# Kernel tuning notes

Measured on AMD Instinct MI355X. Metric: run time of the kernel, lower is better.

## Reference

```python
import jax, jax.numpy as jnp
import numpy as np

E, D, H = 1024, 64, 16   # embed_dim, head_dim, num_heads
B, L = 8, 4096


def _ln(x, g, b, eps=1e-5):
    m = jnp.mean(x, axis=-1, keepdims=True)
    v = jnp.var(x, axis=-1, keepdims=True)
    return (x - m) / jnp.sqrt(v + eps) * g + b


def setup_inputs() -> dict:
    key = jax.random.key(0)
    ks = jax.random.split(key, 10)
    s_e = 1.0 / np.sqrt(E)
    s_d = 1.0 / np.sqrt(D)
    f32 = jnp.float32
    return {
        "emb": jax.random.normal(ks[0], (B, L, E), f32),
        # per-head linears stacked on a leading head axis
        "Wa": jax.random.normal(ks[1], (H, E, D), f32) * s_e,
        "ba": jnp.zeros((H, D), f32),
        "Wb": jax.random.normal(ks[2], (H, E, D), f32) * s_e,
        "bb": jnp.zeros((H, D), f32),
        "Wc": jax.random.normal(ks[3], (H, D, D), f32) * s_d,
        "bc": jnp.zeros((H, D), f32),
        "head_w": jnp.ones((H,), f32),
        "hn_g": jnp.ones((H, D), f32),
        "hn_b": jnp.zeros((H, D), f32),
        "Wd": jax.random.normal(ks[4], (E, D), f32) * s_e,
        "bd": jnp.zeros((D,), f32),
        "W1": jax.random.normal(ks[5], (D, 4 * D), f32) * s_d,
        "b1": jnp.zeros((4 * D,), f32),
        "W2": jax.random.normal(ks[6], (4 * D, D), f32) * (1.0 / np.sqrt(4 * D)),
        "b2": jnp.zeros((D,), f32),
        "Wp": jax.random.normal(ks[7], (D, D), f32) * s_d,
        "bp": jnp.zeros((D,), f32),
        "ng": jnp.ones((D,), f32),
        "nb": jnp.zeros((D,), f32),
    }


def reference(emb, Wa, ba, Wb, bb, Wc, bc, head_w, hn_g, hn_b,
              Wd, bd, W1, b1, W2, b2, Wp, bp, ng, nb):
    b_sz, seq_len, _ = emb.shape
    n_heads, d_head = ba.shape

    # gates depend only on x_t -> precompute for all t, all heads  [B,L,H,D]
    a = jnp.tanh(jnp.einsum('ble,hed->blhd', emb, Wa) + ba)
    bt = jnp.einsum('ble,hed->blhd', emb, Wb) + bb

    # linear recurrence h_t = a_t * h_{t-1} + b_t over time
    a_t = jnp.moveaxis(a, 1, 0)    # [L,B,H,D]
    b_t = jnp.moveaxis(bt, 1, 0)

    def step(h, ab):
        at, btt = ab
        h = at * h + btt
        return h, h

    h0 = jnp.zeros((b_sz, n_heads, d_head), emb.dtype)
    _, hs = jax.lax.scan(step, h0, (a_t, b_t))
    hs = jnp.moveaxis(hs, 0, 1)    # [B,L,H,D]

    dx = emb @ Wd + bd             # [B,L,D] shared D(x_t)

    out = jnp.einsum('blhd,hde->blhe', hs, Wc) + bc + dx[:, :, None, :]
    out = _ln(out, hn_g, hn_b)     # per-head LayerNorm, gamma/beta [H,D]

    sum_heads = dx + jnp.einsum('h,blhd->bld', head_w, out)
    z = sum_heads / n_heads

    u = z + _ln(z, ng, nb)
    ffn = jax.nn.gelu(u @ W1 + b1, approximate=False) @ W2 + b2
    h_out = u + ffn
    return h_out @ Wp + bp
```

## Files before the change

### kernel.cpp

```cpp
#include <hip/hip_runtime.h>
#include <hip/hip_bf16.h>
#include <math.h>
#include <stdint.h>

#define E_DIM 1024
#define D_DIM 64
#define H_DIM 16
#define B_SZ  8
#define L_SEQ 4096
#define M_TOK (B_SZ * L_SEQ)
#define NCAT  2112
#define NPAD  2176
#define CHUNK 128
#define NCHUNK (L_SEQ / CHUNK)

typedef float  f32x4  __attribute__((ext_vector_type(4)));
typedef __bf16 bf16x8 __attribute__((ext_vector_type(8)));
typedef __bf16 bf16x4 __attribute__((ext_vector_type(4)));

__device__ __forceinline__ float tanh_fast(float v) {
  float vc = fminf(fmaxf(v, -12.f), 12.f);
  float ex = __expf(vc + vc);
  return (ex - 1.f) / (ex + 1.f);
}
__device__ __forceinline__ void load_lds16(const void* g, void* l) {
  __builtin_amdgcn_global_load_lds(
      (const __attribute__((address_space(1))) void*)g,
      (__attribute__((address_space(3))) void*)l, 16, 0, 0);
}

__global__ __launch_bounds__(256) void prep(
    const float* __restrict__ emb, bf16x4* __restrict__ embh,
    const float* __restrict__ Wa, const float* __restrict__ ba,
    const float* __restrict__ Wb, const float* __restrict__ bb,
    const float* __restrict__ Wd, const float* __restrict__ bd,
    __bf16* __restrict__ wcat, float* __restrict__ bias,
    const float* __restrict__ W1, const float* __restrict__ W2,
    const float* __restrict__ Wp,
    __bf16* __restrict__ g_w1t, __bf16* __restrict__ g_w2t,
    __bf16* __restrict__ g_wpt,
    const float* __restrict__ Wc, __bf16* __restrict__ wct) {
  const int blk = blockIdx.x, tid = threadIdx.x;
  if (blk < 32768) {
    int i = blk * 256 + tid;
    float4 v = ((const float4*)emb)[i];
    bf16x4 o;
    o[0] = (__bf16)v.x; o[1] = (__bf16)v.y; o[2] = (__bf16)v.z; o[3] = (__bf16)v.w;
    embh[i] = o;
  } else if (blk < 41472) {
    int gid = (blk - 32768) * 256 + tid;
    int n = gid >> 10, k = gid & 1023;
    float w, bv;
    if (n < 1024) {
      int h = n >> 6, d = n & 63;
      w = Wa[((h << 10) | k) * 64 + d]; bv = ba[n];
    } else if (n < 2048) {
      int nn = n - 1024; int h = nn >> 6, d = nn & 63;
      w = Wb[((h << 10) | k) * 64 + d]; bv = bb[nn];
    } else if (n < NCAT) {
      int d = n - 2048;
      w = Wd[k * 64 + d];  bv = bd[d];
    } else { w = 0.f; bv = 0.f; }
    wcat[n * 1024 + k] = (__bf16)w;
    if (k == 0) bias[n] = bv;
  } else if (blk < 41616) {
    int idx = (blk - 41472) * 256 + tid;
    if (idx < 16384) {
      int k = idx >> 8, n = idx & 255;
      g_w1t[n * 72 + k] = (__bf16)W1[idx];
    } else if (idx < 32768) {
      int j = idx - 16384; int k = j >> 6, n = j & 63;
      g_w2t[n * 256 + k] = (__bf16)W2[j];
    } else {
      int j = idx - 32768; int k = j >> 6, n = j & 63;
      g_wpt[n * 72 + k] = (__bf16)Wp[j];
    }
  } else {
    int idx = (blk - 41616) * 256 + tid;
    int h = idx >> 12, e = (idx >> 6) & 63, d = idx & 63;
    wct[idx] = (__bf16)Wc[h * 4096 + d * 64 + e];
  }
}

__global__ __launch_bounds__(256) void gemm_fused(
    const __bf16* __restrict__ A, const __bf16* __restrict__ Wt,
    const float* __restrict__ bias,
    __bf16* __restrict__ abuf, __bf16* __restrict__ bbuf, float* __restrict__ dxbuf) {
  __shared__ __bf16 As[128 * 64];
  __shared__ __bf16 Bs[128 * 64];
  const int bb = blockIdx.x;
  const int xcd = bb & 7, wv = bb >> 3;
  const int nt = wv % 17;
  const int mt = xcd * 32 + wv / 17;
  const int m0 = mt * 128, n0 = nt * 128;
  const int t = threadIdx.x, w = t >> 6, l = t & 63;
  const int lr = l >> 3, lc = l & 7;
  const int swz = lc ^ lr;
  const int q = l >> 4, c16 = l & 15;

  f32x4 acc[4][4];
#pragma unroll
  for (int i = 0; i < 4; ++i)
#pragma unroll
    for (int j = 0; j < 4; ++j) acc[i][j] = (f32x4)(0.f);

  const __bf16* gA = A  + (size_t)(m0 + w * 8 + lr) * 1024 + swz * 8;
  const __bf16* gB = Wt + (size_t)(n0 + w * 8 + lr) * 1024 + swz * 8;
  __bf16* lA = As + w * 512;
  __bf16* lB = Bs + w * 512;

  for (int kk = 0; kk < 16; ++kk) {
    const int k0 = kk * 64;
#pragma unroll
    for (int r = 0; r < 4; ++r) {
      load_lds16(gA + (size_t)r * 32 * 1024 + k0, lA + r * 2048);
      load_lds16(gB + (size_t)r * 32 * 1024 + k0, lB + r * 2048);
    }
    __syncthreads();
#pragma unroll
    for (int ks = 0; ks < 2; ++ks) {
      bf16x8 af[4], bfr[4];
#pragma unroll
      for (int i = 0; i < 4; ++i) {
        int mloc = (w >> 1) * 64 + i * 16 + c16;
        int cp = (ks * 4 + q) ^ (mloc & 7);
        af[i] = *(const bf16x8*)(As + mloc * 64 + cp * 8);
      }
#pragma unroll
      for (int j = 0; j < 4; ++j) {
        int nloc = (w & 1) * 64 + j * 16 + c16;
        int cp = (ks * 4 + q) ^ (nloc & 7);
        bfr[j] = *(const bf16x8*)(Bs + nloc * 64 + cp * 8);
      }
#pragma unroll
      for (int i = 0; i < 4; ++i)
#pragma unroll
        for (int j = 0; j < 4; ++j)
          acc[i][j] = __builtin_amdgcn_mfma_f32_16x16x32_bf16(af[i], bfr[j], acc[i][j], 0, 0, 0);
    }
    __syncthreads();
  }

#pragma unroll
  for (int j = 0; j < 4; ++j) {
    int n = n0 + (w & 1) * 64 + j * 16 + c16;
    float bv = bias[n];
#pragma unroll
    for (int i = 0; i < 4; ++i) {
      int mbase = m0 + (w >> 1) * 64 + i * 16 + q * 4;
#pragma unroll
      for (int r = 0; r < 4; ++r) {
        float v = acc[i][j][r] + bv;
        int m = mbase + r;
        if (n < 1024)            abuf[(size_t)m * 1024 + n] = (__bf16)tanh_fast(v);
        else if (n < 2048)       bbuf[(size_t)m * 1024 + (n - 1024)] = (__bf16)v;
        else if (n < NCAT)       dxbuf[m * 64 + (n - 2048)] = v;
      }
    }
  }
}

__global__ __launch_bounds__(256) void scan_local_bf(
    __bf16* __restrict__ abuf, __bf16* __restrict__ bbuf,
    float* __restrict__ cA, float* __restrict__ cH) {
  int bc = blockIdx.x;
  int n4 = threadIdx.x * 4;
  size_t base = (size_t)bc * CHUNK * 1024 + n4;
  float p[4] = {1.f, 1.f, 1.f, 1.f}, h[4] = {0.f, 0.f, 0.f, 0.f};
  for (int s = 0; s < CHUNK; ++s) {
    size_t idx = base + (size_t)s * 1024;
    bf16x4 av = *(const bf16x4*)(abuf + idx);
    bf16x4 bv = *(const bf16x4*)(bbuf + idx);
    bf16x4 po, ho;
#pragma unroll
    for (int i = 0; i < 4; ++i) {
      float a = (float)av[i];
      p[i] *= a;
      h[i] = fmaf(a, h[i], (float)bv[i]);
      po[i] = (__bf16)p[i];
      ho[i] = (__bf16)h[i];
    }
    *(bf16x4*)(abuf + idx) = po;
    *(bf16x4*)(bbuf + idx) = ho;
  }
  int ci = bc * 1024 + n4;
  float4 pv = {p[0], p[1], p[2], p[3]};
  float4 hv = {h[0], h[1], h[2], h[3]};
  *(float4*)(cA + ci) = pv;
  *(float4*)(cH + ci) = hv;
}

__global__ __launch_bounds__(256) void scan_carry(
    const float* __restrict__ cA, const float* __restrict__ cH, float* __restrict__ cIn) {
  int gid = blockIdx.x * 256 + threadIdx.x;
  int n = gid & 1023, b = gid >> 10;
  float carry = 0.f;
  for (int c = 0; c < NCHUNK; ++c) {
    int idx = (b * NCHUNK + c) * 1024 + n;
    cIn[idx] = carry;
    carry = fmaf(cA[idx], carry, cH[idx]);
  }
}

__global__ __launch_bounds__(256) void heads_mfma(
    const __bf16* __restrict__ ahat, const __bf16* __restrict__ hloc,
    const float* __restrict__ dxbuf, const float* __restrict__ cIn,
    const __bf16* __restrict__ wct, const float* __restrict__ bch,
    const float* __restrict__ head_w, const float* __restrict__ hng,
    const float* __restrict__ hnb, const float* __restrict__ ng,
    const float* __restrict__ nbv, float* __restrict__ ubuf) {
  __shared__ float carryS[1024];
  const int tid = threadIdx.x, w = tid >> 6, l = tid & 63;
  const int q = l >> 4, c16 = l & 15;
  const int m0 = blockIdx.x * 64;
  const int b = m0 >> 12, c = (m0 & 4095) >> 7;
  const int cb = (b * NCHUNK + c) * 1024;
  ((float4*)carryS)[tid] = ((const float4*)(cIn + cb))[tid];
  __syncthreads();

  const size_t arow = (size_t)(m0 + w * 16 + c16) * 1024;

  float dxr[4][4];
#pragma unroll
  for (int j = 0; j < 4; ++j)
#pragma unroll
    for (int r = 0; r < 4; ++r)
      dxr[j][r] = dxbuf[(m0 + w * 16 + q * 4 + r) * 64 + j * 16 + c16];

  f32x4 accum[4];
#pragma unroll
  for (int j = 0; j < 4; ++j) accum[j] = (f32x4)(0.f);

  for (int h = 0; h < H_DIM; ++h) {
    bf16x8 af[2];
#pragma unroll
    for (int ks = 0; ks < 2; ++ks) {
      int dbase = h * 64 + ks * 32 + q * 8;
      bf16x8 av = *(const bf16x8*)(ahat + arow + dbase);
      bf16x8 hv = *(const bf16x8*)(hloc + arow + dbase);
      float4 cv0 = *(const float4*)(carryS + dbase);
      float4 cv1 = *(const float4*)(carryS + dbase + 4);
      bf16x8 hf;
      hf[0] = (__bf16)fmaf((float)av[0], cv0.x, (float)hv[0]);
      hf[1] = (__bf16)fmaf((float)av[1], cv0.y, (float)hv[1]);
      hf[2] = (__bf16)fmaf((float)av[2], cv0.z, (float)hv[2]);
      hf[3] = (__bf16)fmaf((float)av[3], cv0.w, (float)hv[3]);
      hf[4] = (__bf16)fmaf((float)av[4], cv1.x, (float)hv[4]);
      hf[5] = (__bf16)fmaf((float)av[5], cv1.y, (float)hv[5]);
      hf[6] = (__bf16)fmaf((float)av[6], cv1.z, (float)hv[6]);
      hf[7] = (__bf16)fmaf((float)av[7], cv1.w, (float)hv[7]);
      af[ks] = hf;
    }
    f32x4 acc[4];
#pragma unroll
    for (int j = 0; j < 4; ++j) acc[j] = (f32x4)(0.f);
#pragma unroll
    for (int ks = 0; ks < 2; ++ks)
#pragma unroll
      for (int j = 0; j < 4; ++j) {
        bf16x8 bf = *(const bf16x8*)(wct + h * 4096 + (j * 16 + c16) * 64 + ks * 32 + q * 8);
        acc[j] = __builtin_amdgcn_mfma_f32_16x16x32_bf16(af[ks], bf, acc[j], 0, 0, 0);
      }
    float hw = head_w[h];
    float g4[4], be4[4], bb4[4];
#pragma unroll
    for (int j = 0; j < 4; ++j) {
      int nh = h * 64 + j * 16 + c16;
      g4[j] = hng[nh]; bb4[j] = hnb[nh]; be4[j] = bch[nh];
    }
#pragma unroll
    for (int r = 0; r < 4; ++r) {
      float v0 = acc[0][r] + be4[0] + dxr[0][r];
      float v1 = acc[1][r] + be4[1] + dxr[1][r];
      float v2 = acc[2][r] + be4[2] + dxr[2][r];
      float v3 = acc[3][r] + be4[3] + dxr[3][r];
      float s  = (v0 + v1) + (v2 + v3);
      float s2 = fmaf(v0, v0, fmaf(v1, v1, fmaf(v2, v2, v3 * v3)));
#pragma unroll
      for (int off = 1; off < 16; off <<= 1) {
        s  += __shfl_xor(s, off, 64);
        s2 += __shfl_xor(s2, off, 64);
      }
      float mean = s * (1.f / 64.f);
      float var  = fmaf(s2, 1.f / 64.f, -mean * mean);
      float inv  = rsqrtf(fmaxf(var, 0.f) + 1e-5f);
      accum[0][r] = fmaf(hw, fmaf((v0 - mean) * inv, g4[0], bb4[0]), accum[0][r]);
      accum[1][r] = fmaf(hw, fmaf((v1 - mean) * inv, g4[1], bb4[1]), accum[1][r]);
      accum[2][r] = fmaf(hw, fmaf((v2 - mean) * inv, g4[2], bb4[2]), accum[2][r]);
      accum[3][r] = fmaf(hw, fmaf((v3 - mean) * inv, g4[3], bb4[3]), accum[3][r]);
    }
  }
  float ng4[4], nb4[4];
#pragma unroll
  for (int j = 0; j < 4; ++j) { ng4[j] = ng[j * 16 + c16]; nb4[j] = nbv[j * 16 + c16]; }
#pragma unroll
  for (int r = 0; r < 4; ++r) {
    float z0 = (dxr[0][r] + accum[0][r]) * (1.f / 16.f);
    float z1 = (dxr[1][r] + accum[1][r]) * (1.f / 16.f);
    float z2 = (dxr[2][r] + accum[2][r]) * (1.f / 16.f);
    float z3 = (dxr[3][r] + accum[3][r]) * (1.f / 16.f);
    float s  = (z0 + z1) + (z2 + z3);
    float s2 = fmaf(z0, z0, fmaf(z1, z1, fmaf(z2, z2, z3 * z3)));
#pragma unroll
    for (int off = 1; off < 16; off <<= 1) {
      s  += __shfl_xor(s, off, 64);
      s2 += __shfl_xor(s2, off, 64);
    }
    float mean = s * (1.f / 64.f);
    float var  = fmaf(s2, 1.f / 64.f, -mean * mean);
    float inv  = rsqrtf(fmaxf(var, 0.f) + 1e-5f);
    int mrow = (m0 + w * 16 + q * 4 + r) * 64;
    ubuf[mrow + 0 * 16 + c16] = z0 + fmaf((z0 - mean) * inv, ng4[0], nb4[0]);
    ubuf[mrow + 1 * 16 + c16] = z1 + fmaf((z1 - mean) * inv, ng4[1], nb4[1]);
    ubuf[mrow + 2 * 16 + c16] = z2 + fmaf((z2 - mean) * inv, ng4[2], nb4[2]);
    ubuf[mrow + 3 * 16 + c16] = z3 + fmaf((z3 - mean) * inv, ng4[3], nb4[3]);
  }
}

__global__ __launch_bounds__(256) void ffn_wave(
    const float* __restrict__ ubuf,
    const __bf16* __restrict__ g_w1t, const __bf16* __restrict__ g_w2t,
    const __bf16* __restrict__ g_wpt,
    const float* __restrict__ b1, const float* __restrict__ b2,
    const float* __restrict__ bp, float* __restrict__ out) {
  __shared__ __bf16 tls[4][4096];
  const int tid = threadIdx.x, w = tid >> 6, l = tid & 63;
  const int q = l >> 4, c16 = l & 15;
  const int m0w = blockIdx.x * 64 + w * 16;
  __bf16* T = tls[w];

  bf16x8 ua[2];
#pragma unroll
  for (int ks = 0; ks < 2; ++ks) {
    const float* up = ubuf + (size_t)(m0w + c16) * 64 + ks * 32 + q * 8;
    float4 v0 = *(const float4*)up;
    float4 v1 = *(const float4*)(up + 4);
    bf16x8 tt;
    tt[0] = (__bf16)v0.x; tt[1] = (__bf16)v0.y; tt[2] = (__bf16)v0.z; tt[3] = (__bf16)v0.w;
    tt[4] = (__bf16)v1.x; tt[5] = (__bf16)v1.y; tt[6] = (__bf16)v1.z; tt[7] = (__bf16)v1.w;
    ua[ks] = tt;
  }

  f32x4 acc1[16];
#pragma unroll
  for (int j = 0; j < 16; ++j) acc1[j] = (f32x4)(0.f);
#pragma unroll
  for (int j = 0; j < 16; ++j) {
    const __bf16* bp1 = g_w1t + (j * 16 + c16) * 72 + q * 8;
    bf16x8 b0 = *(const bf16x8*)bp1;
    bf16x8 b1f = *(const bf16x8*)(bp1 + 32);
    acc1[j] = __builtin_amdgcn_mfma_f32_16x16x32_bf16(ua[0], b0, acc1[j], 0, 0, 0);
    acc1[j] = __builtin_amdgcn_mfma_f32_16x16x32_bf16(ua[1], b1f, acc1[j], 0, 0, 0);
  }

#pragma unroll
  for (int j = 0; j < 16; ++j) {
    int n = j * 16 + c16;
    float bv = b1[n];
#pragma unroll
    for (int rr = 0; rr < 4; ++rr) {
      int tok = q * 4 + rr;
      float x = acc1[j][rr] + bv;
      float g = 0.5f * x * (1.f + erff(x * 0.70710678118654752f));
      T[tok * 256 + (((n >> 3) ^ (tok & 7)) << 3) + (n & 7)] = (__bf16)g;
    }
  }
  __builtin_amdgcn_wave_barrier();

  f32x4 acc2[4];
#pragma unroll
  for (int j = 0; j < 4; ++j) acc2[j] = (f32x4)(0.f);
#pragma unroll
  for (int ks = 0; ks < 8; ++ks) {
    bf16x8 a = *(const bf16x8*)(T + c16 * 256 + (((ks * 4 + q) ^ (c16 & 7)) << 3));
#pragma unroll
    for (int j = 0; j < 4; ++j) {
      bf16x8 b = *(const bf16x8*)(g_w2t + (j * 16 + c16) * 256 + ks * 32 + q * 8);
      acc2[j] = __builtin_amdgcn_mfma_f32_16x16x32_bf16(a, b, acc2[j], 0, 0, 0);
    }
  }
  __builtin_amdgcn_wave_barrier();

#pragma unroll
  for (int j = 0; j < 4; ++j) {
    int e = j * 16 + c16;
    float bv = b2[e];
#pragma unroll
    for (int rr = 0; rr < 4; ++rr) {
      int tok = q * 4 + rr;
      float hres = acc2[j][rr] + bv + ubuf[(size_t)(m0w + tok) * 64 + e];
      T[tok * 64 + (((e >> 3) ^ (tok & 7)) << 3) + (e & 7)] = (__bf16)hres;
    }
  }
  __builtin_amdgcn_wave_barrier();

  f32x4 acc3[4];
#pragma unroll
  for (int j = 0; j < 4; ++j) acc3[j] = (f32x4)(0.f);
#pragma unroll
  for (int ks = 0; ks < 2; ++ks) {
    bf16x8 a = *(const bf16x8*)(T + c16 * 64 + (((ks * 4 + q) ^ (c16 & 7)) << 3));
#pragma unroll
    for (int j = 0; j < 4; ++j) {
      bf16x8 b = *(const bf16x8*)(g_wpt + (j * 16 + c16) * 72 + ks * 32 + q * 8);
      acc3[j] = __builtin_amdgcn_mfma_f32_16x16x32_bf16(a, b, acc3[j], 0, 0, 0);
    }
  }
#pragma unroll
  for (int j = 0; j < 4; ++j) {
    int e = j * 16 + c16;
    float bv = bp[e];
#pragma unroll
    for (int rr = 0; rr < 4; ++rr)
      out[(size_t)(m0w + q * 4 + rr) * 64 + e] = acc3[j][rr] + bv;
  }
}

extern "C" void kernel_launch(void* const* d_in, const int* in_sizes, int n_in,
                              void* d_out, int out_size, void* d_ws, size_t ws_size,
                              hipStream_t stream) {
  const float* emb    = (const float*)d_in[0];
  const float* Wa     = (const float*)d_in[1];
  const float* ba     = (const float*)d_in[2];
  const float* Wb     = (const float*)d_in[3];
  const float* bb     = (const float*)d_in[4];
  const float* Wc     = (const float*)d_in[5];
  const float* bc     = (const float*)d_in[6];
  const float* head_w = (const float*)d_in[7];
  const float* hn_g   = (const float*)d_in[8];
  const float* hn_b   = (const float*)d_in[9];
  const float* Wd     = (const float*)d_in[10];
  const float* bd     = (const float*)d_in[11];
  const float* W1     = (const float*)d_in[12];
  const float* b1     = (const float*)d_in[13];
  const float* W2     = (const float*)d_in[14];
  const float* b2     = (const float*)d_in[15];
  const float* Wp     = (const float*)d_in[16];
  const float* bp     = (const float*)d_in[17];
  const float* ng     = (const float*)d_in[18];
  const float* nb     = (const float*)d_in[19];
  float* out = (float*)d_out;

  char* wsp = (char*)d_ws;
  size_t off = 0;
  auto alloc = [&](size_t bytes) -> char* {
    char* p = wsp + off;
    off += (bytes + 255) & ~(size_t)255;
    return p;
  };
  __bf16* embh  = (__bf16*)alloc((size_t)M_TOK * E_DIM * 2);
  __bf16* wcat  = (__bf16*)alloc((size_t)NPAD * E_DIM * 2);
  float*  bias  = (float*)alloc((size_t)NPAD * 4);
  __bf16* abuf  = (__bf16*)alloc((size_t)M_TOK * 1024 * 2);
  __bf16* bbuf  = (__bf16*)alloc((size_t)M_TOK * 1024 * 2);
  float*  dxbuf = (float*)alloc((size_t)M_TOK * 64 * 4);
  float*  cA    = (float*)alloc((size_t)256 * 1024 * 4);
  float*  cH    = (float*)alloc((size_t)256 * 1024 * 4);
  float*  cIn   = (float*)alloc((size_t)256 * 1024 * 4);
  float*  ubuf  = (float*)alloc((size_t)M_TOK * 64 * 4);
  __bf16* g_w1t = (__bf16*)alloc((size_t)256 * 72 * 2);
  __bf16* g_w2t = (__bf16*)alloc((size_t)64 * 256 * 2);
  __bf16* g_wpt = (__bf16*)alloc((size_t)64 * 72 * 2);
  __bf16* wct   = (__bf16*)alloc((size_t)H_DIM * 64 * 64 * 2);

  prep<<<dim3(41872), dim3(256), 0, stream>>>(
      emb, (bf16x4*)embh, Wa, ba, Wb, bb, Wd, bd, wcat, bias,
      W1, W2, Wp, g_w1t, g_w2t, g_wpt, Wc, wct);
  gemm_fused<<<dim3(4352), dim3(256), 0, stream>>>(embh, wcat, bias, abuf, bbuf, dxbuf);
  scan_local_bf<<<dim3(256), dim3(256), 0, stream>>>(abuf, bbuf, cA, cH);
  scan_carry<<<dim3(32), dim3(256), 0, stream>>>(cA, cH, cIn);
  heads_mfma<<<dim3(512), dim3(256), 0, stream>>>(abuf, bbuf, dxbuf, cIn, wct, bc,
                                                  head_w, hn_g, hn_b, ng, nb, ubuf);
  ffn_wave<<<dim3(512), dim3(256), 0, stream>>>(ubuf, g_w1t, g_w2t, g_wpt,
                                                b1, b2, bp, out);
}
```

Baseline: 610.9 us.

## Fuse carry scan, heads and FFN into one kernel; load GEMM B fragments directly

Removes the scan_carry kernel by having each heads block recompute its chunk carry from the per-chunk (A,H) summaries. It also merges heads_mfma and ffn_wave so the u tensor stays in registers and LDS and never round-trips through global memory. The main GEMM now reads B-operand fragments straight from global memory into registers instead of staging them through LDS, which halves the shared memory used and drops the B-side LDS traffic. The cost is redundant carry work (up to 31 chunk steps per block), more registers per thread in the fused kernel, and B-operand global loads that are no longer shared across waves.

Result: slower. 718.2 us (+17.6%).

```diff
diff --git a/kernel.cpp b/kernel.cpp
--- a/kernel.cpp
+++ b/kernel.cpp
@@ -87,7 +87,6 @@
     const float* __restrict__ bias,
     __bf16* __restrict__ abuf, __bf16* __restrict__ bbuf, float* __restrict__ dxbuf) {
   __shared__ __bf16 As[128 * 64];
-  __shared__ __bf16 Bs[128 * 64];
   const int bb = blockIdx.x;
   const int xcd = bb & 7, wv = bb >> 3;
   const int nt = wv % 17;
@@ -104,22 +103,31 @@
 #pragma unroll
     for (int j = 0; j < 4; ++j) acc[i][j] = (f32x4)(0.f);
 
-  const __bf16* gA = A  + (size_t)(m0 + w * 8 + lr) * 1024 + swz * 8;
-  const __bf16* gB = Wt + (size_t)(n0 + w * 8 + lr) * 1024 + swz * 8;
+  const __bf16* gA = A + (size_t)(m0 + w * 8 + lr) * 1024 + swz * 8;
   __bf16* lA = As + w * 512;
-  __bf16* lB = Bs + w * 512;
+
+  const __bf16* gBj[4];
+#pragma unroll
+  for (int j = 0; j < 4; ++j)
+    gBj[j] = Wt + (size_t)(n0 + (w & 1) * 64 + j * 16 + c16) * 1024 + q * 8;
 
   for (int kk = 0; kk < 16; ++kk) {
     const int k0 = kk * 64;
 #pragma unroll
-    for (int r = 0; r < 4; ++r) {
+    for (int r = 0; r < 4; ++r)
       load_lds16(gA + (size_t)r * 32 * 1024 + k0, lA + r * 2048);
-      load_lds16(gB + (size_t)r * 32 * 1024 + k0, lB + r * 2048);
-    }
+
+    bf16x8 bfr[2][4];
+#pragma unroll
+    for (int ks = 0; ks < 2; ++ks)
+#pragma unroll
+      for (int j = 0; j < 4; ++j)
+        bfr[ks][j] = *(const bf16x8*)(gBj[j] + k0 + ks * 32);
+
     __syncthreads();
 #pragma unroll
     for (int ks = 0; ks < 2; ++ks) {
-      bf16x8 af[4], bfr[4];
+      bf16x8 af[4];
 #pragma unroll
       for (int i = 0; i < 4; ++i) {
         int mloc = (w >> 1) * 64 + i * 16 + c16;
@@ -127,16 +135,10 @@
         af[i] = *(const bf16x8*)(As + mloc * 64 + cp * 8);
       }
 #pragma unroll
-      for (int j = 0; j < 4; ++j) {
-        int nloc = (w & 1) * 64 + j * 16 + c16;
-        int cp = (ks * 4 + q) ^ (nloc & 7);
-        bfr[j] = *(const bf16x8*)(Bs + nloc * 64 + cp * 8);
-      }
-#pragma unroll
       for (int i = 0; i < 4; ++i)
 #pragma unroll
         for (int j = 0; j < 4; ++j)
-          acc[i][j] = __builtin_amdgcn_mfma_f32_16x16x32_bf16(af[i], bfr[j], acc[i][j], 0, 0, 0);
+          acc[i][j] = __builtin_amdgcn_mfma_f32_16x16x32_bf16(af[i], bfr[ks][j], acc[i][j], 0, 0, 0);
     }
     __syncthreads();
   }
@@ -190,32 +192,38 @@
   *(float4*)(cH + ci) = hv;
 }
 
-__global__ __launch_bounds__(256) void scan_carry(
-    const float* __restrict__ cA, const float* __restrict__ cH, float* __restrict__ cIn) {
-  int gid = blockIdx.x * 256 + threadIdx.x;
-  int n = gid & 1023, b = gid >> 10;
-  float carry = 0.f;
-  for (int c = 0; c < NCHUNK; ++c) {
-    int idx = (b * NCHUNK + c) * 1024 + n;
-    cIn[idx] = carry;
-    carry = fmaf(cA[idx], carry, cH[idx]);
-  }
-}
-
-__global__ __launch_bounds__(256) void heads_mfma(
+__global__ __launch_bounds__(256) void heads_ffn(
     const __bf16* __restrict__ ahat, const __bf16* __restrict__ hloc,
-    const float* __restrict__ dxbuf, const float* __restrict__ cIn,
-    const __bf16* __restrict__ wct, const float* __restrict__ bch,
-    const float* __restrict__ head_w, const float* __restrict__ hng,
-    const float* __restrict__ hnb, const float* __restrict__ ng,
-    const float* __restrict__ nbv, float* __restrict__ ubuf) {
+    const float* __restrict__ dxbuf, const float* __restrict__ cA,
+    const float* __restrict__ cH, const __bf16* __restrict__ wct,
+    const float* __restrict__ bch, const float* __restrict__ head_w,
+    const float* __restrict__ hng, const float* __restrict__ hnb,
+    const float* __restrict__ ng, const float* __restrict__ nbv,
+    const __bf16* __restrict__ g_w1t, const __bf16* __restrict__ g_w2t,
+    const __bf16* __restrict__ g_wpt,
+    const float* __restrict__ b1, const float* __restrict__ b2,
+    const float* __restrict__ bp, float* __restrict__ out) {
   __shared__ float carryS[1024];
+  __shared__ __bf16 tls[4][4096];
   const int tid = threadIdx.x, w = tid >> 6, l = tid & 63;
   const int q = l >> 4, c16 = l & 15;
   const int m0 = blockIdx.x * 64;
   const int b = m0 >> 12, c = (m0 & 4095) >> 7;
-  const int cb = (b * NCHUNK + c) * 1024;
-  ((float4*)carryS)[tid] = ((const float4*)(cIn + cb))[tid];
+
+  {
+    float4 carry = {0.f, 0.f, 0.f, 0.f};
+    const int n4 = tid * 4;
+    for (int cc = 0; cc < c; ++cc) {
+      int ci = (b * NCHUNK + cc) * 1024 + n4;
+      float4 A4 = *(const float4*)(cA + ci);
+      float4 H4 = *(const float4*)(cH + ci);
+      carry.x = fmaf(A4.x, carry.x, H4.x);
+      carry.y = fmaf(A4.y, carry.y, H4.y);
+      carry.z = fmaf(A4.z, carry.z, H4.z);
+      carry.w = fmaf(A4.w, carry.w, H4.w);
+    }
+    *(float4*)(carryS + n4) = carry;
+  }
   __syncthreads();
 
   const size_t arow = (size_t)(m0 + w * 16 + c16) * 1024;
@@ -290,56 +298,51 @@
       accum[3][r] = fmaf(hw, fmaf((v3 - mean) * inv, g4[3], bb4[3]), accum[3][r]);
     }
   }
-  float ng4[4], nb4[4];
-#pragma unroll
-  for (int j = 0; j < 4; ++j) { ng4[j] = ng[j * 16 + c16]; nb4[j] = nbv[j * 16 + c16]; }
-#pragma unroll
-  for (int r = 0; r < 4; ++r) {
-    float z0 = (dxr[0][r] + accum[0][r]) * (1.f / 16.f);
-    float z1 = (dxr[1][r] + accum[1][r]) * (1.f / 16.f);
-    float z2 = (dxr[2][r] + accum[2][r]) * (1.f / 16.f);
-    float z3 = (dxr[3][r] + accum[3][r]) * (1.f / 16.f);
-    float s  = (z0 + z1) + (z2 + z3);
-    float s2 = fmaf(z0, z0, fmaf(z1, z1, fmaf(z2, z2, z3 * z3)));
-#pragma unroll
-    for (int off = 1; off < 16; off <<= 1) {
-      s  += __shfl_xor(s, off, 64);
-      s2 += __shfl_xor(s2, off, 64);
-    }
-    float mean = s * (1.f / 64.f);
-    float var  = fmaf(s2, 1.f / 64.f, -mean * mean);
-    float inv  = rsqrtf(fmaxf(var, 0.f) + 1e-5f);
-    int mrow = (m0 + w * 16 + q * 4 + r) * 64;
-    ubuf[mrow + 0 * 16 + c16] = z0 + fmaf((z0 - mean) * inv, ng4[0], nb4[0]);
-    ubuf[mrow + 1 * 16 + c16] = z1 + fmaf((z1 - mean) * inv, ng4[1], nb4[1]);
-    ubuf[mrow + 2 * 16 + c16] = z2 + fmaf((z2 - mean) * inv, ng4[2], nb4[2]);
-    ubuf[mrow + 3 * 16 + c16] = z3 + fmaf((z3 - mean) * inv, ng4[3], nb4[3]);
-  }
-}
-
-__global__ __launch_bounds__(256) void ffn_wave(
-    const float* __restrict__ ubuf,
-    const __bf16* __restrict__ g_w1t, const __bf16* __restrict__ g_w2t,
-    const __bf16* __restrict__ g_wpt,
-    const float* __restrict__ b1, const float* __restrict__ b2,
-    const float* __restrict__ bp, float* __restrict__ out) {
-  __shared__ __bf16 tls[4][4096];
-  const int tid = threadIdx.x, w = tid >> 6, l = tid & 63;
-  const int q = l >> 4, c16 = l & 15;
-  const int m0w = blockIdx.x * 64 + w * 16;
+
+  float uC[4][4];
+  {
+    float ng4[4], nb4[4];
+#pragma unroll
+    for (int j = 0; j < 4; ++j) { ng4[j] = ng[j * 16 + c16]; nb4[j] = nbv[j * 16 + c16]; }
+#pragma unroll
+    for (int r = 0; r < 4; ++r) {
+      float z0 = (dxr[0][r] + accum[0][r]) * (1.f / 16.f);
+      float z1 = (dxr[1][r] + accum[1][r]) * (1.f / 16.f);
+      float z2 = (dxr[2][r] + accum[2][r]) * (1.f / 16.f);
+      float z3 = (dxr[3][r] + accum[3][r]) * (1.f / 16.f);
+      float s  = (z0 + z1) + (z2 + z3);
+      float s2 = fmaf(z0, z0, fmaf(z1, z1, fmaf(z2, z2, z3 * z3)));
+#pragma unroll
+      for (int off = 1; off < 16; off <<= 1) {
+        s  += __shfl_xor(s, off, 64);
+        s2 += __shfl_xor(s2, off, 64);
+      }
+      float mean = s * (1.f / 64.f);
+      float var  = fmaf(s2, 1.f / 64.f, -mean * mean);
+      float inv  = rsqrtf(fmaxf(var, 0.f) + 1e-5f);
+      uC[0][r] = z0 + fmaf((z0 - mean) * inv, ng4[0], nb4[0]);
+      uC[1][r] = z1 + fmaf((z1 - mean) * inv, ng4[1], nb4[1]);
+      uC[2][r] = z2 + fmaf((z2 - mean) * inv, ng4[2], nb4[2]);
+      uC[3][r] = z3 + fmaf((z3 - mean) * inv, ng4[3], nb4[3]);
+    }
+  }
+
   __bf16* T = tls[w];
-
+#pragma unroll
+  for (int j = 0; j < 4; ++j) {
+    int e = j * 16 + c16;
+#pragma unroll
+    for (int r = 0; r < 4; ++r) {
+      int tok = q * 4 + r;
+      T[tok * 64 + (((e >> 3) ^ (tok & 7)) << 3) + (e & 7)] = (__bf16)uC[j][r];
+    }
+  }
+  __builtin_amdgcn_wave_barrier();
   bf16x8 ua[2];
 #pragma unroll
-  for (int ks = 0; ks < 2; ++ks) {
-    const float* up = ubuf + (size_t)(m0w + c16) * 64 + ks * 32 + q * 8;
-    float4 v0 = *(const float4*)up;
-    float4 v1 = *(const float4*)(up + 4);
-    bf16x8 tt;
-    tt[0] = (__bf16)v0.x; tt[1] = (__bf16)v0.y; tt[2] = (__bf16)v0.z; tt[3] = (__bf16)v0.w;
-    tt[4] = (__bf16)v1.x; tt[5] = (__bf16)v1.y; tt[6] = (__bf16)v1.z; tt[7] = (__bf16)v1.w;
-    ua[ks] = tt;
-  }
+  for (int ks = 0; ks < 2; ++ks)
+    ua[ks] = *(const bf16x8*)(T + c16 * 64 + (((ks * 4 + q) ^ (c16 & 7)) << 3));
+  __builtin_amdgcn_wave_barrier();
 
   f32x4 acc1[16];
 #pragma unroll
@@ -352,7 +355,6 @@
     acc1[j] = __builtin_amdgcn_mfma_f32_16x16x32_bf16(ua[0], b0, acc1[j], 0, 0, 0);
     acc1[j] = __builtin_amdgcn_mfma_f32_16x16x32_bf16(ua[1], b1f, acc1[j], 0, 0, 0);
   }
-
 #pragma unroll
   for (int j = 0; j < 16; ++j) {
     int n = j * 16 + c16;
@@ -375,8 +377,8 @@
     bf16x8 a = *(const bf16x8*)(T + c16 * 256 + (((ks * 4 + q) ^ (c16 & 7)) << 3));
 #pragma unroll
     for (int j = 0; j < 4; ++j) {
-      bf16x8 b = *(const bf16x8*)(g_w2t + (j * 16 + c16) * 256 + ks * 32 + q * 8);
-      acc2[j] = __builtin_amdgcn_mfma_f32_16x16x32_bf16(a, b, acc2[j], 0, 0, 0);
+      bf16x8 bf = *(const bf16x8*)(g_w2t + (j * 16 + c16) * 256 + ks * 32 + q * 8);
+      acc2[j] = __builtin_amdgcn_mfma_f32_16x16x32_bf16(a, bf, acc2[j], 0, 0, 0);
     }
   }
   __builtin_amdgcn_wave_barrier();
@@ -388,7 +390,7 @@
 #pragma unroll
     for (int rr = 0; rr < 4; ++rr) {
       int tok = q * 4 + rr;
-      float hres = acc2[j][rr] + bv + ubuf[(size_t)(m0w + tok) * 64 + e];
+      float hres = acc2[j][rr] + bv + uC[j][rr];
       T[tok * 64 + (((e >> 3) ^ (tok & 7)) << 3) + (e & 7)] = (__bf16)hres;
     }
   }
@@ -402,8 +404,8 @@
     bf16x8 a = *(const bf16x8*)(T + c16 * 64 + (((ks * 4 + q) ^ (c16 & 7)) << 3));
 #pragma unroll
     for (int j = 0; j < 4; ++j) {
-      bf16x8 b = *(const bf16x8*)(g_wpt + (j * 16 + c16) * 72 + ks * 32 + q * 8);
-      acc3[j] = __builtin_amdgcn_mfma_f32_16x16x32_bf16(a, b, acc3[j], 0, 0, 0);
+      bf16x8 bf = *(const bf16x8*)(g_wpt + (j * 16 + c16) * 72 + ks * 32 + q * 8);
+      acc3[j] = __builtin_amdgcn_mfma_f32_16x16x32_bf16(a, bf, acc3[j], 0, 0, 0);
     }
   }
 #pragma unroll
@@ -412,7 +414,7 @@
     float bv = bp[e];
 #pragma unroll
     for (int rr = 0; rr < 4; ++rr)
-      out[(size_t)(m0w + q * 4 + rr) * 64 + e] = acc3[j][rr] + bv;
+      out[(size_t)(m0 + w * 16 + q * 4 + rr) * 64 + e] = acc3[j][rr] + bv;
   }
 }
 
@@ -456,8 +458,6 @@
   float*  dxbuf = (float*)alloc((size_t)M_TOK * 64 * 4);
   float*  cA    = (float*)alloc((size_t)256 * 1024 * 4);
   float*  cH    = (float*)alloc((size_t)256 * 1024 * 4);
-  float*  cIn   = (float*)alloc((size_t)256 * 1024 * 4);
-  float*  ubuf  = (float*)alloc((size_t)M_TOK * 64 * 4);
   __bf16* g_w1t = (__bf16*)alloc((size_t)256 * 72 * 2);
   __bf16* g_w2t = (__bf16*)alloc((size_t)64 * 256 * 2);
   __bf16* g_wpt = (__bf16*)alloc((size_t)64 * 72 * 2);
@@ -468,9 +468,7 @@
       W1, W2, Wp, g_w1t, g_w2t, g_wpt, Wc, wct);
   gemm_fused<<<dim3(4352), dim3(256), 0, stream>>>(embh, wcat, bias, abuf, bbuf, dxbuf);
   scan_local_bf<<<dim3(256), dim3(256), 0, stream>>>(abuf, bbuf, cA, cH);
-  scan_carry<<<dim3(32), dim3(256), 0, stream>>>(cA, cH, cIn);
-  heads_mfma<<<dim3(512), dim3(256), 0, stream>>>(abuf, bbuf, dxbuf, cIn, wct, bc,
-                                                  head_w, hn_g, hn_b, ng, nb, ubuf);
-  ffn_wave<<<dim3(512), dim3(256), 0, stream>>>(ubuf, g_w1t, g_w2t, g_wpt,
-                                                b1, b2, bp, out);
-}
+  heads_ffn<<<dim3(512), dim3(256), 0, stream>>>(abuf, bbuf, dxbuf, cA, cH, wct, bc,
+                                                 head_w, hn_g, hn_b, ng, nb,
+                                                 g_w1t, g_w2t, g_wpt, b1, b2, bp, out);
+}
```
